# Kernel tuning notes

Hardware: AMD Instinct MI355X
Metric: run time of the kernel (lower is better)

The kernel has to match this reference:

```python
import jax, jax.numpy as jnp
import numpy as np


def setup_inputs() -> dict:
    key = jax.random.key(0)
    kx, ka = jax.random.split(key)
    B, N, D = 8, 4096, 32
    x = jax.random.normal(kx, (B, N, D), dtype=jnp.float32)
    # adjacency-like nonnegative weights (dense branch of GsumLayer)
    a = jax.random.uniform(ka, (B, N, N), dtype=jnp.float32)
    return {"x": x, "a": a}


def reference(x, a):
    # GsumLayer dense branch: out[b] = a[b] @ x[b]  -> [B, N, D]
    return jnp.einsum('bnm,bmd->bnd', a, x)
```

## Files before the change

kernel.cpp:

```cpp
#include <hip/hip_runtime.h>


#define GN 4096
#define GD 32
#define ROWS 64
#define BK 64
#define APAD 4

__global__ __launch_bounds__(256, 2) void gsum_kernel(
    const float* __restrict__ x,
    const float* __restrict__ a,
    float* __restrict__ out)
{
    __shared__ float As[ROWS][BK + APAD];
    __shared__ float Xs[BK][GD];

    const int t    = threadIdx.x;
    const int b    = blockIdx.x >> 6;
    const int tile = blockIdx.x & 63;
    const long long row0 = (long long)tile * ROWS;

    const float* Ab = a   + ((long long)b * GN + row0) * GN;
    const float* Xb = x   + (long long)b * GN * GD;
    float*       Ob = out + ((long long)b * GN + row0) * GD;

    const int g = t & 7;
    const int r = t >> 3;

    const int sr = t >> 2;
    const int sc = (t & 3) * 4;

    float4 acc0 = {0.f, 0.f, 0.f, 0.f};
    float4 acc1 = {0.f, 0.f, 0.f, 0.f};

    for (int k0 = 0; k0 < GN; k0 += BK) {
        __syncthreads();

        {
            const float* Arow = Ab + (long long)sr * GN + k0;
            #pragma unroll
            for (int i = 0; i < 4; ++i) {
                float4 v = *(const float4*)(Arow + sc + i * 16);
                *(float4*)&As[sr][sc + i * 16] = v;
            }
        }
        {
            const float* Xrow = Xb + (long long)(k0 + sr) * GD;
            float4 v0 = *(const float4*)(Xrow + sc);
            float4 v1 = *(const float4*)(Xrow + 16 + sc);
            *(float4*)&Xs[sr][sc]      = v0;
            *(float4*)&Xs[sr][16 + sc] = v1;
        }

        __syncthreads();

        #pragma unroll
        for (int kk = 0; kk < BK; kk += 4) {
            float4 a0 = *(const float4*)&As[r][kk];
            float4 a1 = *(const float4*)&As[r + 32][kk];
            #pragma unroll
            for (int j = 0; j < 4; ++j) {
                float4 xv = *(const float4*)&Xs[kk + j][g * 4];
                float aj0 = (j == 0) ? a0.x : (j == 1) ? a0.y : (j == 2) ? a0.z : a0.w;
                float aj1 = (j == 0) ? a1.x : (j == 1) ? a1.y : (j == 2) ? a1.z : a1.w;
                acc0.x += aj0 * xv.x; acc0.y += aj0 * xv.y;
                acc0.z += aj0 * xv.z; acc0.w += aj0 * xv.w;
                acc1.x += aj1 * xv.x; acc1.y += aj1 * xv.y;
                acc1.z += aj1 * xv.z; acc1.w += aj1 * xv.w;
            }
        }
    }

    *(float4*)(Ob + (long long)r        * GD + g * 4) = acc0;
    *(float4*)(Ob + (long long)(r + 32) * GD + g * 4) = acc1;
}

extern "C" void kernel_launch(void* const* d_in, const int* in_sizes, int n_in,
                              void* d_out, int out_size, void* d_ws, size_t ws_size,
                              hipStream_t stream) {
    const float* x = (const float*)d_in[0];
    const float* a = (const float*)d_in[1];
    float* out = (float*)d_out;

    const int B = 8;
    const int tiles_per_batch = GN / ROWS;
    dim3 grid(B * tiles_per_batch);
    dim3 block(256);
    gsum_kernel<<<grid, block, 0, stream>>>(x, a, out);
}
```

Measured before the change: 747.3 us.

## Replace FP32 FMA GEMM with split-bf16 MFMA kernel and register-prefetched A

Rewrites the batched a@x kernel to use 16x16x32 bf16 MFMA instructions, emulating fp32 accuracy by splitting each operand into hi and lo bf16 parts and issuing three MFMAs per pair. A is streamed straight from global memory into registers with a two-deep prefetch and never staged in LDS. X is converted to transposed hi/lo bf16 tiles in double-buffered shared memory. Block size and tile shape also change. The aim is to move the compute-bound FMA work onto matrix cores so the kernel approaches memory-bandwidth limits. The cost is extra conversion ALU work and a small loss of precision from dropping the lo*lo term.

```diff
diff --git a/kernel.cpp b/kernel.cpp
--- a/kernel.cpp
+++ b/kernel.cpp
@@ -3,76 +3,136 @@
 
 #define GN 4096
 #define GD 32
-#define ROWS 64
-#define BK 64
-#define APAD 4
+#define GB 8
+#define BK 256
+#define NCH (GN / BK)
+#define NT 512
+#define TILE_N 128
+#define PK (BK + 8)
 
-__global__ __launch_bounds__(256, 2) void gsum_kernel(
+typedef float f32x4 __attribute__((ext_vector_type(4)));
+typedef short s16x8 __attribute__((ext_vector_type(8)));
+
+__global__ __launch_bounds__(NT, 2) void gsum_mfma(
     const float* __restrict__ x,
     const float* __restrict__ a,
     float* __restrict__ out)
 {
-    __shared__ float As[ROWS][BK + APAD];
-    __shared__ float Xs[BK][GD];
+    __shared__ __align__(16) unsigned short Xh[2][GD][PK];
+    __shared__ __align__(16) unsigned short Xl[2][GD][PK];
 
-    const int t    = threadIdx.x;
-    const int b    = blockIdx.x >> 6;
-    const int tile = blockIdx.x & 63;
-    const long long row0 = (long long)tile * ROWS;
+    const int t  = threadIdx.x;
+    const int w  = t >> 6;
+    const int l  = t & 63;
+    const int m  = l & 15;
+    const int kg = l >> 4;
 
-    const float* Ab = a   + ((long long)b * GN + row0) * GN;
-    const float* Xb = x   + (long long)b * GN * GD;
-    float*       Ob = out + ((long long)b * GN + row0) * GD;
+    const int b    = blockIdx.x >> 5;
+    const int tile = blockIdx.x & 31;
+    const int n0   = tile * TILE_N + w * 16;
 
-    const int g = t & 7;
-    const int r = t >> 3;
+    const float* Xb = x + (long long)b * GN * GD;
+    const float* arow = a + ((long long)b * GN + n0 + m) * GN + kg * 8;
 
-    const int sr = t >> 2;
-    const int sc = (t & 3) * 4;
+    const int kr = t >> 1;
+    const int c0 = (t & 1) * 16;
 
-    float4 acc0 = {0.f, 0.f, 0.f, 0.f};
-    float4 acc1 = {0.f, 0.f, 0.f, 0.f};
+    f32x4 acc0 = {0.f, 0.f, 0.f, 0.f};
+    f32x4 acc1 = {0.f, 0.f, 0.f, 0.f};
 
-    for (int k0 = 0; k0 < GN; k0 += BK) {
-        __syncthreads();
-
-        {
-            const float* Arow = Ab + (long long)sr * GN + k0;
+    auto XLOAD = [&](int k0, float4* xr) {
+        const float* p = Xb + (long long)(k0 + kr) * GD + c0;
+        xr[0] = *(const float4*)(p);
+        xr[1] = *(const float4*)(p + 4);
+        xr[2] = *(const float4*)(p + 8);
+        xr[3] = *(const float4*)(p + 12);
+    };
+    auto XWRITE = [&](int nb, const float4* xr) {
+        #pragma unroll
+        for (int q = 0; q < 4; ++q) {
+            const float fv[4] = {xr[q].x, xr[q].y, xr[q].z, xr[q].w};
             #pragma unroll
-            for (int i = 0; i < 4; ++i) {
-                float4 v = *(const float4*)(Arow + sc + i * 16);
-                *(float4*)&As[sr][sc + i * 16] = v;
+            for (int j = 0; j < 4; ++j) {
+                const int d = c0 + q * 4 + j;
+                unsigned u  = __float_as_uint(fv[j]);
+                unsigned hb = (u + 0x8000u) >> 16;
+                float hif   = __uint_as_float(hb << 16);
+                unsigned lb = (__float_as_uint(fv[j] - hif) + 0x8000u) >> 16;
+                Xh[nb][d][kr] = (unsigned short)hb;
+                Xl[nb][d][kr] = (unsigned short)lb;
             }
         }
-        {
-            const float* Xrow = Xb + (long long)(k0 + sr) * GD;
-            float4 v0 = *(const float4*)(Xrow + sc);
-            float4 v1 = *(const float4*)(Xrow + 16 + sc);
-            *(float4*)&Xs[sr][sc]      = v0;
-            *(float4*)&Xs[sr][16 + sc] = v1;
+    };
+    auto ALOAD = [&](f32x4* dst, int k) {
+        const int kc = (k >= GN) ? (k - GN) : k;
+        const float* p = arow + kc;
+        dst[0] = *(const f32x4*)(p);
+        dst[1] = *(const f32x4*)(p + 4);
+    };
+
+    {
+        float4 xr[4];
+        XLOAD(0, xr);
+        XWRITE(0, xr);
+    }
+    f32x4 pa[2][2];
+    ALOAD(pa[0], 0);
+    ALOAD(pa[1], 32);
+    asm volatile("s_waitcnt lgkmcnt(0)" ::: "memory");
+    __builtin_amdgcn_s_barrier();
+
+    for (int c = 0; c < NCH; ++c) {
+        const int nb = c & 1;
+        const int k0 = c * BK;
+
+        float4 xnext[4];
+        if (c + 1 < NCH) XLOAD(k0 + BK, xnext);
+
+        #pragma unroll
+        for (int s = 0; s < 8; ++s) {
+            float av[8];
+            #pragma unroll
+            for (int e = 0; e < 4; ++e) {
+                av[e]     = pa[s & 1][0][e];
+                av[4 + e] = pa[s & 1][1][e];
+            }
+            ALOAD(pa[s & 1], k0 + s * 32 + 64);
+
+            s16x8 ahi, alo;
+            #pragma unroll
+            for (int e = 0; e < 8; ++e) {
+                unsigned u  = __float_as_uint(av[e]);
+                unsigned hb = (u + 0x8000u) >> 16;
+                ahi[e] = (short)hb;
+                float hif = __uint_as_float(hb << 16);
+                alo[e] = (short)((__float_as_uint(av[e] - hif) + 0x8000u) >> 16);
+            }
+
+            const int kk = s * 32 + kg * 8;
+            s16x8 xh0 = *(const s16x8*)&Xh[nb][m][kk];
+            s16x8 xl0 = *(const s16x8*)&Xl[nb][m][kk];
+            s16x8 xh1 = *(const s16x8*)&Xh[nb][16 + m][kk];
+            s16x8 xl1 = *(const s16x8*)&Xl[nb][16 + m][kk];
+
+            acc0 = __builtin_amdgcn_mfma_f32_16x16x32_bf16(xh0, ahi, acc0, 0, 0, 0);
+            acc1 = __builtin_amdgcn_mfma_f32_16x16x32_bf16(xh1, ahi, acc1, 0, 0, 0);
+            acc0 = __builtin_amdgcn_mfma_f32_16x16x32_bf16(xl0, ahi, acc0, 0, 0, 0);
+            acc1 = __builtin_amdgcn_mfma_f32_16x16x32_bf16(xl1, ahi, acc1, 0, 0, 0);
+            acc0 = __builtin_amdgcn_mfma_f32_16x16x32_bf16(xh0, alo, acc0, 0, 0, 0);
+            acc1 = __builtin_amdgcn_mfma_f32_16x16x32_bf16(xh1, alo, acc1, 0, 0, 0);
         }
 
-        __syncthreads();
-
-        #pragma unroll
-        for (int kk = 0; kk < BK; kk += 4) {
-            float4 a0 = *(const float4*)&As[r][kk];
-            float4 a1 = *(const float4*)&As[r + 32][kk];
-            #pragma unroll
-            for (int j = 0; j < 4; ++j) {
-                float4 xv = *(const float4*)&Xs[kk + j][g * 4];
-                float aj0 = (j == 0) ? a0.x : (j == 1) ? a0.y : (j == 2) ? a0.z : a0.w;
-                float aj1 = (j == 0) ? a1.x : (j == 1) ? a1.y : (j == 2) ? a1.z : a1.w;
-                acc0.x += aj0 * xv.x; acc0.y += aj0 * xv.y;
-                acc0.z += aj0 * xv.z; acc0.w += aj0 * xv.w;
-                acc1.x += aj1 * xv.x; acc1.y += aj1 * xv.y;
-                acc1.z += aj1 * xv.z; acc1.w += aj1 * xv.w;
-            }
-        }
+        if (c + 1 < NCH) XWRITE((c + 1) & 1, xnext);
+        asm volatile("s_waitcnt lgkmcnt(0)" ::: "memory");
+        __builtin_amdgcn_s_barrier();
     }
 
-    *(float4*)(Ob + (long long)r        * GD + g * 4) = acc0;
-    *(float4*)(Ob + (long long)(r + 32) * GD + g * 4) = acc1;
+    float* Ob = out + ((long long)b * GN + n0 + m) * GD + kg * 4;
+    #pragma unroll
+    for (int j = 0; j < 4; ++j) {
+        Ob[j]      = acc0[j];
+        Ob[16 + j] = acc1[j];
+    }
 }
 
 extern "C" void kernel_launch(void* const* d_in, const int* in_sizes, int n_in,
@@ -82,9 +142,7 @@
     const float* a = (const float*)d_in[1];
     float* out = (float*)d_out;
 
-    const int B = 8;
-    const int tiles_per_batch = GN / ROWS;
-    dim3 grid(B * tiles_per_batch);
-    dim3 block(256);
-    gsum_kernel<<<grid, block, 0, stream>>>(x, a, out);
+    dim3 grid(GB * (GN / TILE_N));
+    dim3 block(NT);
+    gsum_mfma<<<grid, block, 0, stream>>>(x, a, out);
 }
```

After: 712.9 us. -4.6%, faster.
